# Kernel optimization log

Hardware: AMD Instinct MI355X
Metric: run time of the kernel (lower is better)

Reference implementation:

```python
import math
import jax, jax.numpy as jnp
import numpy as np

B, N, D_FULL, M, D_V = 8, 4096, 256, 256, 256


def _phi(x, omega):
    # x: [..., N, d_full], omega: [M, d_full] -> [..., N, M]
    proj = x @ omega.T
    log_phi = proj - 0.5 * jnp.sum(x * x, axis=-1, keepdims=True)
    log_phi = log_phi - jnp.max(log_phi, axis=-1, keepdims=True)
    return jnp.exp(log_phi) / math.sqrt(omega.shape[0])


def _causal(phi_q, phi_k, V):
    # phi_q/phi_k: [B, N, M], V: [B, N, d_v]
    b, n, m = phi_q.shape
    d_v = V.shape[-1]

    def step(carry, inp):
        S, z = carry
        pq, pk, v = inp  # [B,M], [B,M], [B,d_v]
        S = S + pk[:, :, None] * v[:, None, :]          # [B, M, d_v]
        z = z + pk                                       # [B, M]
        num = jnp.einsum('bi,bij->bj', pq, S)            # [B, d_v]
        den = jnp.maximum(jnp.sum(pq * z, axis=-1), 1e-6)
        return (S, z), num / den[:, None]

    S0 = jnp.zeros((b, m, d_v), phi_q.dtype)
    z0 = jnp.zeros((b, m), phi_q.dtype)
    xs = (jnp.swapaxes(phi_q, 0, 1), jnp.swapaxes(phi_k, 0, 1), jnp.swapaxes(V, 0, 1))
    _, ys = jax.lax.scan(step, (S0, z0), xs)  # ys: [N, B, d_v]
    return jnp.swapaxes(ys, 0, 1)


def setup_inputs() -> dict:
    key = jax.random.key(0)
    kq, kk, kv, ko = jax.random.split(key, 4)
    Q = jax.random.normal(kq, (B, N, D_FULL), dtype=jnp.float32)
    K_in = jax.random.normal(kk, (B, N, D_FULL), dtype=jnp.float32)
    V = jax.random.normal(kv, (B, N, D_V), dtype=jnp.float32)
    omega = jax.random.normal(ko, (M, D_FULL), dtype=jnp.float32)
    return {"Q": Q, "K_in": K_in, "V": V, "omega": omega, "causal": 1}


def reference(Q, K_in, V, omega, causal):
    phi_q = _phi(Q, omega)
    phi_k = _phi(K_in, omega)
    if causal:
        return _causal(phi_q, phi_k, V)
    S = jnp.einsum('bni,bnj->bij', phi_k, V)          # [B, M, d_v]
    z = jnp.sum(phi_k, axis=-2)                        # [B, M]
    num = jnp.einsum('bni,bij->bnj', phi_q, S)
    den = jnp.maximum(jnp.einsum('bni,bi->bn', phi_q, z), 1e-6)
    return num / den[..., None]
```

## Files before the change

kernel.cpp:

```cpp
#include <hip/hip_runtime.h>

#define BN 8
#define NN 4096
#define DD 256
#define MM 256
#define DV 256
#define CHUNK 256
#define NC (NN / CHUNK)

using f32x4 = __attribute__((ext_vector_type(4))) float;
using s16x8 = __attribute__((ext_vector_type(8))) short;

#define MFMA16(a, b, c) __builtin_amdgcn_mfma_f32_16x16x32_bf16(a, b, c, 0, 0, 0)


__device__ __forceinline__ unsigned short f2bf(float x) {
    union { float f; unsigned int u; } v; v.f = x;
    unsigned int r = v.u + 0x7FFF + ((v.u >> 16) & 1);
    return (unsigned short)(r >> 16);
}
__device__ __forceinline__ float bf2f(unsigned short u) {
    union { unsigned int u; float f; } v; v.u = ((unsigned int)u) << 16;
    return v.f;
}

__device__ __forceinline__ void split4(const float4 x, unsigned short h[4], unsigned short l[4])
{
    const float xs[4] = {x.x, x.y, x.z, x.w};
#pragma unroll
    for (int j = 0; j < 4; ++j) {
        union { float f; unsigned u; } v; v.f = xs[j];
        const unsigned hm = v.u & 0xFFFF0000u;
        union { unsigned u; float f; } hv; hv.u = hm;
        h[j] = (unsigned short)(hm >> 16);
        l[j] = f2bf(xs[j] - hv.f);
    }
}

__global__ __launch_bounds__(256) void omconv(
    const float* __restrict__ Om, unsigned short* __restrict__ OmH,
    unsigned short* __restrict__ OmL)
{
    const int i = blockIdx.x * 256 + threadIdx.x;
    const int row = i >> 6;
    const int k0  = (i & 63) * 4;
    const float4 v = *(const float4*)(Om + (size_t)row * DD + k0);
    const int wv = row >> 6, ct = (row >> 4) & 3, colL = row & 15;
    const int kt = k0 >> 5, quad = (k0 >> 3) & 3, e0 = k0 & 7;
    const int lanep = quad * 16 + colL;
    const size_t off = ((size_t)((wv * 8 + kt) * 4 + ct) * 64 + lanep) * 8 + e0;
    unsigned short h[4], l[4];
    split4(v, h, l);
    *(uint2*)(OmH + off) = *(uint2*)h;
    *(uint2*)(OmL + off) = *(uint2*)l;
}

__global__ __launch_bounds__(256, 4) void phi_fused(
    const float* __restrict__ Qp, const float* __restrict__ Kp,
    const float* __restrict__ Vp,
    const unsigned short* __restrict__ OmH, const unsigned short* __restrict__ OmL,
    unsigned short* __restrict__ PhiQF, unsigned short* __restrict__ PhiKF,
    unsigned short* __restrict__ PhiTF, unsigned short* __restrict__ VTF,
    float* __restrict__ Zp)
{
    const int tid = threadIdx.x;
    const int w = tid >> 6;
    const int lane = tid & 63;
    const int col = lane & 15, quad = lane >> 4;

    __shared__ __align__(16) short AhS[32][264];
    __shared__ __align__(16) short AlS[32][264];
    __shared__ float rowmax_s[32];
    float (*red)[68] = (float(*)[68])AhS;
    unsigned short (*P)[264] = (unsigned short(*)[264])AlS;
    unsigned int* P32 = (unsigned int*)AlS;

    if (blockIdx.x >= 2048) {
        const int vid = blockIdx.x - 2048;
        const int ct = vid & 3;
        const long r0v = (long)(vid >> 2) * 64;
        const int b = (int)(r0v >> 12);
        const int n0 = (int)(r0v & (NN - 1));
        const int c = n0 >> 8;
        const int kt0 = (n0 & 255) >> 5;
        const size_t bcv = ((size_t)(b * NC + c)) << 16;
        unsigned short (*T)[72] = (unsigned short(*)[72])AhS;
        const int rr = tid >> 4, cs = tid & 15;
#pragma unroll
        for (int p = 0; p < 4; ++p) {
            const int r = p * 16 + rr;
            const float4 v = *(const float4*)(Vp + (r0v + r) * DV + ct * 64 + cs * 4);
            T[cs * 4 + 0][r] = f2bf(v.x); T[cs * 4 + 1][r] = f2bf(v.y);
            T[cs * 4 + 2][r] = f2bf(v.z); T[cs * 4 + 3][r] = f2bf(v.w);
        }
        __syncthreads();
#pragma unroll
        for (int p = 0; p < 2; ++p) {
            const uint4 v = *(const uint4*)&T[w * 16 + col][p * 32 + quad * 8];
            *(uint4*)(VTF + bcv + (((size_t)(ct * 8 + kt0 + p) * 4 + w) * 64 + lane) * 8) = v;
        }
        return;
    }

    const bool kpath = blockIdx.x < 1024;
    const int id = kpath ? blockIdx.x : (blockIdx.x - 1024);
    const float* __restrict__ X = kpath ? Kp : Qp;
    const long r0 = (long)id * 32;

    {
        float4 xv[8];
#pragma unroll
        for (int j = 0; j < 8; ++j) {
            const int row = w * 8 + j;
            xv[j] = *(const float4*)(X + (r0 + row) * DD + lane * 4);
        }
#pragma unroll
        for (int j = 0; j < 8; ++j) {
            const int row = w * 8 + j;
            unsigned short h[4], l[4];
            split4(xv[j], h, l);
            *(uint2*)&AhS[row][lane * 4] = *(uint2*)h;
            *(uint2*)&AlS[row][lane * 4] = *(uint2*)l;
        }
    }

    const unsigned short* OmHw = OmH + (size_t)w * 8 * 4 * 512;
    const unsigned short* OmLw = OmL + (size_t)w * 8 * 4 * 512;
    f32x4 acc[2][4] = {};
    s16x8 bh0[4], bl0[4], bh1[4], bl1[4];
#pragma unroll
    for (int ct = 0; ct < 4; ++ct) {
        const size_t off = ((size_t)ct * 64 + lane) * 8;
        bh0[ct] = *(const s16x8*)(OmHw + off);
        bl0[ct] = *(const s16x8*)(OmLw + off);
    }
    __syncthreads();

#pragma unroll
    for (int kt = 0; kt < 8; ++kt) {
        if (kt < 7) {
#pragma unroll
            for (int ct = 0; ct < 4; ++ct) {
                const size_t off = ((size_t)((kt + 1) * 4 + ct) * 64 + lane) * 8;
                bh1[ct] = *(const s16x8*)(OmHw + off);
                bl1[ct] = *(const s16x8*)(OmLw + off);
            }
        }
#pragma unroll
        for (int t = 0; t < 2; ++t) {
            const s16x8 ah = *(const s16x8*)&AhS[t * 16 + col][kt * 32 + quad * 8];
            const s16x8 al = *(const s16x8*)&AlS[t * 16 + col][kt * 32 + quad * 8];
#pragma unroll
            for (int ct = 0; ct < 4; ++ct) {
                acc[t][ct] = MFMA16(ah, bh0[ct], acc[t][ct]);
                acc[t][ct] = MFMA16(ah, bl0[ct], acc[t][ct]);
                acc[t][ct] = MFMA16(al, bh0[ct], acc[t][ct]);
            }
        }
#pragma unroll
        for (int ct = 0; ct < 4; ++ct) { bh0[ct] = bh1[ct]; bl0[ct] = bl1[ct]; }
    }

    __syncthreads();
#pragma unroll
    for (int t = 0; t < 2; ++t)
#pragma unroll
        for (int r = 0; r < 4; ++r) {
            float m = acc[t][0][r];
#pragma unroll
            for (int ct = 1; ct < 4; ++ct) m = fmaxf(m, acc[t][ct][r]);
            red[t * 16 + quad * 4 + r][w * 16 + col] = m;
        }
    __syncthreads();
    {
        const int row = tid >> 3, seg = tid & 7;
        float m = red[row][seg * 8];
#pragma unroll
        for (int j = 1; j < 8; ++j) m = fmaxf(m, red[row][seg * 8 + j]);
        m = fmaxf(m, __shfl_xor(m, 1));
        m = fmaxf(m, __shfl_xor(m, 2));
        m = fmaxf(m, __shfl_xor(m, 4));
        if (seg == 0) rowmax_s[row] = m;
    }
    __syncthreads();

#pragma unroll
    for (int t = 0; t < 2; ++t)
#pragma unroll
        for (int r = 0; r < 4; ++r) {
            const int n = t * 16 + quad * 4 + r;
            const float rm = rowmax_s[n];
#pragma unroll
            for (int ct = 0; ct < 4; ++ct) {
                const float val = __expf(acc[t][ct][r] - rm) * 0.0625f;
                const unsigned u = (unsigned)f2bf(val);
                const unsigned up = (unsigned)__shfl_xor((int)u, 1);
                if ((col & 1) == 0)
                    P32[n * 132 + w * 32 + ct * 8 + (col >> 1)] = u | (up << 16);
            }
        }
    __syncthreads();

    {
        const int b = id >> 7;
        const int ib = id & 127;
        const int c = ib >> 3;
        const size_t bc = ((size_t)(b * NC + c)) << 16;
        const int jt = (ib >> 1) & 3;
        const int half = ib & 1;
        unsigned short* __restrict__ PF = kpath ? PhiKF : PhiQF;
#pragma unroll
        for (int p = 0; p < 4; ++p) {
            const int msw = p * 4 + w;
            const int ms = msw >> 1, wl = msw & 1;
            const uint4 v = *(const uint4*)&P[wl * 16 + col][ms * 32 + quad * 8];
            *(uint4*)(PF + bc + (((size_t)(jt * 8 + ms) * 4 + half * 2 + wl) * 64 + lane) * 8) = v;
        }
        if (kpath) {
            const int ktp = ib & 7;
#pragma unroll
            for (int p = 0; p < 4; ++p) {
                const int mq = p;
                unsigned short u[8];
#pragma unroll
                for (int e = 0; e < 8; ++e)
                    u[e] = P[quad * 8 + e][mq * 64 + w * 16 + col];
                *(uint4*)(PhiTF + bc + (((size_t)(mq * 8 + ktp) * 4 + w) * 64 + lane) * 8) = *(uint4*)u;
            }
            float z = 0.f;
#pragma unroll
            for (int n = 0; n < 32; ++n) z += bf2f(P[n][tid]);
            atomicAdd(&Zp[((b * NC + c) << 8) + tid], z);
        }
    }
}

__global__ __launch_bounds__(256, 3) void state_mfma(
    const unsigned short* __restrict__ VTF, const unsigned short* __restrict__ PhiTF,
    unsigned short* __restrict__ STF)
{
    const int tid = threadIdx.x;
    const int w = tid >> 6;
    const int lane = tid & 63;
    const int col = lane & 15, quad = lane >> 4;
    const int q  = blockIdx.x >> 7;
    const int bci = blockIdx.x & 127;
    const int c  = bci & 15;
    const int b  = bci >> 4;
    const int dvq = (q & 1) * 2 + (w & 1);
    const int mq  = (q >> 1) * 2 + (w >> 1);
    const size_t bc = ((size_t)(b * NC + c)) << 16;
    const unsigned short* Af = VTF   + bc + (size_t)dvq * 16384;
    const unsigned short* Bf = PhiTF + bc + (size_t)mq  * 16384;

    f32x4 acc[4][4] = {};
    s16x8 a0[4], b0[4], a1[4], b1[4];
#pragma unroll
    for (int t = 0; t < 4; ++t) {
        a0[t] = *(const s16x8*)(Af + ((size_t)t * 64 + lane) * 8);
        b0[t] = *(const s16x8*)(Bf + ((size_t)t * 64 + lane) * 8);
    }
#pragma unroll
    for (int kt = 0; kt < 8; ++kt) {
        if (kt < 7) {
#pragma unroll
            for (int t = 0; t < 4; ++t) {
                a1[t] = *(const s16x8*)(Af + ((size_t)((kt + 1) * 4 + t) * 64 + lane) * 8);
                b1[t] = *(const s16x8*)(Bf + ((size_t)((kt + 1) * 4 + t) * 64 + lane) * 8);
            }
        }
#pragma unroll
        for (int i = 0; i < 4; ++i)
#pragma unroll
            for (int j = 0; j < 4; ++j) acc[i][j] = MFMA16(b0[i], a0[j], acc[i][j]);
#pragma unroll
        for (int t = 0; t < 4; ++t) { a0[t] = a1[t]; b0[t] = b1[t]; }
    }
#pragma unroll
    for (int i = 0; i < 4; ++i)
#pragma unroll
        for (int j = 0; j < 4; ++j) {
            unsigned short s[4];
#pragma unroll
            for (int r = 0; r < 4; ++r) s[r] = f2bf(acc[i][j][r]);
            const int lanep = ((i & 1) * 2 + (quad >> 1)) * 16 + col;
            const size_t off = (((size_t)(dvq * 8 + mq * 2 + (i >> 1)) * 4 + j) * 64 + lanep) * 8 + (quad & 1) * 4;
            *(uint2*)(STF + bc + off) = *(uint2*)s;
        }
}

__global__ __launch_bounds__(256) void prefix2(
    unsigned short* __restrict__ ST, float* __restrict__ Z)
{
    const long idx = (long)blockIdx.x * 256 + threadIdx.x;
    const int b = (int)(idx >> 16);
    const int r = (int)(idx & 65535);
    float run = 0.f;
#pragma unroll
    for (int c = 0; c < NC; ++c) {
        const size_t off = (((size_t)(b * NC + c)) << 16) + r;
        const float v = bf2f(ST[off]);
        ST[off] = f2bf(run);
        run += v;
    }
    if (idx < BN * MM) {
        const int b2 = (int)(idx >> 8);
        const int m = (int)(idx & 255);
        float rz = 0.f;
#pragma unroll
        for (int c = 0; c < NC; ++c) {
            const size_t off = (size_t)(b2 * NC + c) * MM + m;
            const float v = Z[off];
            Z[off] = rz;
            rz += v;
        }
    }
}

__global__ __launch_bounds__(256) void out_mfma(
    const unsigned short* __restrict__ PhiQF, const unsigned short* __restrict__ PhiKF,
    const unsigned short* __restrict__ VTF, const unsigned short* __restrict__ STF,
    const float* __restrict__ Z, float* __restrict__ Out)
{
    const int tid = threadIdx.x;
    const int w = tid >> 6;
    const int lane = tid & 63;
    const int col = lane & 15, quad = lane >> 4;
    const int it = 3 - (blockIdx.x >> 7);
    const int low = blockIdx.x & 127;
    const int c  = low & 15;
    const int b  = low >> 4;
    const size_t chunk_row = (size_t)b * NN + (size_t)c * CHUNK;
    const size_t bc = ((size_t)(b * NC + c)) << 16;
    const unsigned short* Qf = PhiQF + bc + (size_t)it * 16384;
    const unsigned short* Vf = VTF + bc + (size_t)w * 16384;
    const unsigned short* Sf = STF + bc + (size_t)w * 16384;

    __shared__ unsigned short A_s[64][72];
    __shared__ float red[64][20];
    __shared__ float z_s[256];
    __shared__ float den_s[64];

    z_s[tid] = Z[(bc >> 8) + tid];

    f32x4 oacc[4][4] = {};
    float rsum[4][4] = {};

    for (int jt = 0; jt <= it; ++jt) {
        f32x4 accA[4] = {};
#pragma unroll
        for (int ms = 0; ms < 8; ++ms) {
            const s16x8 bk = *(const s16x8*)(PhiKF + bc + (((size_t)(jt * 8 + ms) * 4 + w) * 64 + lane) * 8);
            s16x8 aq[4];
#pragma unroll
            for (int t = 0; t < 4; ++t)
                aq[t] = *(const s16x8*)(Qf + (((size_t)ms * 4 + t) * 64 + lane) * 8);
#pragma unroll
            for (int t = 0; t < 4; ++t)
                accA[t] = MFMA16(aq[t], bk, accA[t]);
        }
        __syncthreads();
#pragma unroll
        for (int t = 0; t < 4; ++t)
#pragma unroll
            for (int r = 0; r < 4; ++r) {
                const int i_loc = t * 16 + quad * 4 + r;
                const int j_loc = w * 16 + col;
                float v = (jt * 64 + j_loc <= it * 64 + i_loc) ? accA[t][r] : 0.f;
                rsum[t][r] += v;
                A_s[i_loc][j_loc] = f2bf(v);
            }
        __syncthreads();
#pragma unroll
        for (int ks2 = 0; ks2 < 2; ++ks2) {
            s16x8 bv[4];
#pragma unroll
            for (int t2 = 0; t2 < 4; ++t2)
                bv[t2] = *(const s16x8*)(Vf + (((size_t)(jt * 2 + ks2) * 4 + t2) * 64 + lane) * 8);
            s16x8 av[4];
#pragma unroll
            for (int t = 0; t < 4; ++t)
                av[t] = *(const s16x8*)&A_s[t * 16 + col][ks2 * 32 + quad * 8];
#pragma unroll
            for (int t2 = 0; t2 < 4; ++t2)
#pragma unroll
                for (int t = 0; t < 4; ++t)
                    oacc[t][t2] = MFMA16(av[t], bv[t2], oacc[t][t2]);
        }
    }

#pragma unroll
    for (int t = 0; t < 4; ++t)
#pragma unroll
        for (int r = 0; r < 4; ++r) {
            float v = rsum[t][r];
            v += __shfl_xor(v, 1);
            v += __shfl_xor(v, 2);
            v += __shfl_xor(v, 4);
            v += __shfl_xor(v, 8);
            if (col == 0) red[t * 16 + quad * 4 + r][w] = v;
        }

    float dpart[4] = {0.f, 0.f, 0.f, 0.f};
#pragma unroll
    for (int ms = 0; ms < 8; ++ms) {
        s16x8 bs[4], aq[4];
#pragma unroll
        for (int t2 = 0; t2 < 4; ++t2)
            bs[t2] = *(const s16x8*)(Sf + (((size_t)ms * 4 + t2) * 64 + lane) * 8);
#pragma unroll
        for (int t = 0; t < 4; ++t)
            aq[t] = *(const s16x8*)(Qf + (((size_t)ms * 4 + t) * 64 + lane) * 8);
#pragma unroll
        for (int t2 = 0; t2 < 4; ++t2)
#pragma unroll
            for (int t = 0; t < 4; ++t)
                oacc[t][t2] = MFMA16(aq[t], bs[t2], oacc[t][t2]);
        if ((ms >> 1) == w) {
#pragma unroll
            for (int t = 0; t < 4; ++t)
#pragma unroll
                for (int e = 0; e < 8; ++e)
                    dpart[t] = fmaf(bf2f((unsigned short)aq[t][e]),
                                    z_s[ms * 32 + quad * 8 + e], dpart[t]);
        }
    }
#pragma unroll
    for (int t = 0; t < 4; ++t)
        red[t * 16 + col][4 + w * 4 + quad] = dpart[t];
    __syncthreads();
    if (tid < 64) {
        float s = 0.f;
#pragma unroll
        for (int j = 0; j < 20; ++j) s += red[tid][j];
        den_s[tid] = fmaxf(s, 1e-6f);
    }
    __syncthreads();
#pragma unroll
    for (int t = 0; t < 4; ++t)
#pragma unroll
        for (int r = 0; r < 4; ++r) {
            const int i_loc = t * 16 + quad * 4 + r;
            const float invd = 1.0f / den_s[i_loc];
#pragma unroll
            for (int t2 = 0; t2 < 4; ++t2)
                Out[(chunk_row + it * 64 + i_loc) * DV + w * 64 + t2 * 16 + col] = oacc[t][t2][r] * invd;
        }
}

extern "C" void kernel_launch(void* const* d_in, const int* in_sizes, int n_in,
                              void* d_out, int out_size, void* d_ws, size_t ws_size,
                              hipStream_t stream)
{
    const float* Q  = (const float*)d_in[0];
    const float* K  = (const float*)d_in[1];
    const float* V  = (const float*)d_in[2];
    const float* Om = (const float*)d_in[3];
    float* out = (float*)d_out;

    const size_t NM = (size_t)BN * NN * MM;
    unsigned short* PhiQF = (unsigned short*)d_ws;
    unsigned short* PhiKF = PhiQF + NM;
    unsigned short* PhiTF = PhiKF + NM;
    unsigned short* VTF   = PhiTF + NM;
    unsigned short* STF   = VTF + NM;
    unsigned short* OmH   = STF + (size_t)BN * NC * DV * MM;
    unsigned short* OmL   = OmH + (size_t)MM * DD;
    float* Z = (float*)(OmL + (size_t)MM * DD);

    hipMemsetAsync(Z, 0, (size_t)BN * NC * MM * sizeof(float), stream);
    omconv<<<dim3(64), dim3(256), 0, stream>>>(Om, OmH, OmL);
    phi_fused<<<dim3(4096), dim3(256), 0, stream>>>(Q, K, V, OmH, OmL, PhiQF, PhiKF, PhiTF, VTF, Z);
    state_mfma<<<dim3(BN * NC * 4), dim3(256), 0, stream>>>(VTF, PhiTF, STF);
    prefix2<<<dim3((BN * DV * MM) / 256), dim3(256), 0, stream>>>(STF, Z);
    out_mfma<<<dim3(BN * NC * 4), dim3(256), 0, stream>>>(PhiQF, PhiKF, VTF, STF, Z, out);
}
```

Baseline: 223.9 us.

## Split phi K-dimension into two halves to halve LDS footprint and overlap loads

The phi_fused kernel now stages the bf16 hi/lo split of the input rows in two halves of 128 columns each, so the shared A buffers shrink from 32x264 to 32x136 per plane. The second half's global loads are issued before the first half's MFMA loop, which overlaps them with compute. The aim is to lower LDS use per block so more blocks can be resident, and to hide load latency. In exchange it adds two extra barriers and loads of half the width, and the held float2 registers may raise register pressure. The aliased reduction and P buffers, of up to 32x264 shorts, must still fit in the 8704-short buffer.

Measured after the change: 223.3 us. About the same (-0.3%).

```diff
diff --git a/kernel.cpp b/kernel.cpp
--- a/kernel.cpp
+++ b/kernel.cpp
@@ -35,6 +35,16 @@
         h[j] = (unsigned short)(hm >> 16);
         l[j] = f2bf(xs[j] - hv.f);
     }
+}
+
+__device__ __forceinline__ void split2(const float2 x, unsigned& hw, unsigned& lw)
+{
+    union { float f; unsigned u; } a, b; a.f = x.x; b.f = x.y;
+    const unsigned ha = a.u & 0xFFFF0000u, hb = b.u & 0xFFFF0000u;
+    union { unsigned u; float f; } fa, fb; fa.u = ha; fb.u = hb;
+    const unsigned la = f2bf(x.x - fa.f), lb = f2bf(x.y - fb.f);
+    hw = (ha >> 16) | hb;
+    lw = (unsigned)la | ((unsigned)lb << 16);
 }
 
 __global__ __launch_bounds__(256) void omconv(
@@ -68,12 +78,13 @@
     const int lane = tid & 63;
     const int col = lane & 15, quad = lane >> 4;
 
-    __shared__ __align__(16) short AhS[32][264];
-    __shared__ __align__(16) short AlS[32][264];
+    __shared__ __align__(16) short BUF[8704];
     __shared__ float rowmax_s[32];
-    float (*red)[68] = (float(*)[68])AhS;
-    unsigned short (*P)[264] = (unsigned short(*)[264])AlS;
-    unsigned int* P32 = (unsigned int*)AlS;
+    short (*AhS)[136] = (short(*)[136])BUF;
+    short (*AlS)[136] = (short(*)[136])(BUF + 4352);
+    float (*red)[68] = (float(*)[68])BUF;
+    unsigned short (*P)[264] = (unsigned short(*)[264])BUF;
+    unsigned int* P32 = (unsigned int*)BUF;
 
     if (blockIdx.x >= 2048) {
         const int vid = blockIdx.x - 2048;
@@ -84,7 +95,7 @@
         const int c = n0 >> 8;
         const int kt0 = (n0 & 255) >> 5;
         const size_t bcv = ((size_t)(b * NC + c)) << 16;
-        unsigned short (*T)[72] = (unsigned short(*)[72])AhS;
+        unsigned short (*T)[72] = (unsigned short(*)[72])BUF;
         const int rr = tid >> 4, cs = tid & 15;
 #pragma unroll
         for (int p = 0; p < 4; ++p) {
@@ -108,21 +119,22 @@
     const long r0 = (long)id * 32;
 
     {
-        float4 xv[8];
+        float2 xv0[8];
+#pragma unroll
+        for (int j = 0; j < 8; ++j)
+            xv0[j] = *(const float2*)(X + (r0 + w * 8 + j) * DD + lane * 2);
 #pragma unroll
         for (int j = 0; j < 8; ++j) {
-            const int row = w * 8 + j;
-            xv[j] = *(const float4*)(X + (r0 + row) * DD + lane * 4);
-        }
-#pragma unroll
-        for (int j = 0; j < 8; ++j) {
-            const int row = w * 8 + j;
-            unsigned short h[4], l[4];
-            split4(xv[j], h, l);
-            *(uint2*)&AhS[row][lane * 4] = *(uint2*)h;
-            *(uint2*)&AlS[row][lane * 4] = *(uint2*)l;
-        }
-    }
+            unsigned hw, lw;
+            split2(xv0[j], hw, lw);
+            *(unsigned*)&AhS[w * 8 + j][lane * 2] = hw;
+            *(unsigned*)&AlS[w * 8 + j][lane * 2] = lw;
+        }
+    }
+    float2 xv1[8];
+#pragma unroll
+    for (int j = 0; j < 8; ++j)
+        xv1[j] = *(const float2*)(X + (r0 + w * 8 + j) * DD + 128 + lane * 2);
 
     const unsigned short* OmHw = OmH + (size_t)w * 8 * 4 * 512;
     const unsigned short* OmLw = OmL + (size_t)w * 8 * 4 * 512;
@@ -137,7 +149,38 @@
     __syncthreads();
 
 #pragma unroll
-    for (int kt = 0; kt < 8; ++kt) {
+    for (int kt = 0; kt < 4; ++kt) {
+#pragma unroll
+        for (int ct = 0; ct < 4; ++ct) {
+            const size_t off = ((size_t)((kt + 1) * 4 + ct) * 64 + lane) * 8;
+            bh1[ct] = *(const s16x8*)(OmHw + off);
+            bl1[ct] = *(const s16x8*)(OmLw + off);
+        }
+#pragma unroll
+        for (int t = 0; t < 2; ++t) {
+            const s16x8 ah = *(const s16x8*)&AhS[t * 16 + col][kt * 32 + quad * 8];
+            const s16x8 al = *(const s16x8*)&AlS[t * 16 + col][kt * 32 + quad * 8];
+#pragma unroll
+            for (int ct = 0; ct < 4; ++ct) {
+                acc[t][ct] = MFMA16(ah, bh0[ct], acc[t][ct]);
+                acc[t][ct] = MFMA16(ah, bl0[ct], acc[t][ct]);
+                acc[t][ct] = MFMA16(al, bh0[ct], acc[t][ct]);
+            }
+        }
+#pragma unroll
+        for (int ct = 0; ct < 4; ++ct) { bh0[ct] = bh1[ct]; bl0[ct] = bl1[ct]; }
+    }
+    __syncthreads();
+#pragma unroll
+    for (int j = 0; j < 8; ++j) {
+        unsigned hw, lw;
+        split2(xv1[j], hw, lw);
+        *(unsigned*)&AhS[w * 8 + j][lane * 2] = hw;
+        *(unsigned*)&AlS[w * 8 + j][lane * 2] = lw;
+    }
+    __syncthreads();
+#pragma unroll
+    for (int kt = 4; kt < 8; ++kt) {
         if (kt < 7) {
 #pragma unroll
             for (int ct = 0; ct < 4; ++ct) {
@@ -148,8 +191,8 @@
         }
 #pragma unroll
         for (int t = 0; t < 2; ++t) {
-            const s16x8 ah = *(const s16x8*)&AhS[t * 16 + col][kt * 32 + quad * 8];
-            const s16x8 al = *(const s16x8*)&AlS[t * 16 + col][kt * 32 + quad * 8];
+            const s16x8 ah = *(const s16x8*)&AhS[t * 16 + col][(kt - 4) * 32 + quad * 8];
+            const s16x8 al = *(const s16x8*)&AlS[t * 16 + col][(kt - 4) * 32 + quad * 8];
 #pragma unroll
             for (int ct = 0; ct < 4; ++ct) {
                 acc[t][ct] = MFMA16(ah, bh0[ct], acc[t][ct]);
```
